# Performance work log

Measured on AMD Instinct MI355X. Metric: run time of the kernel, lower is better.

## Reference

```python
import jax, jax.numpy as jnp
import numpy as np

N_HEADS = 12
LN_EPS = 1e-12


def _attention(x, mask, wq, bq, wk, bk, wv, bv, wo, bo):
    # standard BERT self-attention block (QKV + output projection, no LN here)
    B, S, D = x.shape
    Dh = D // N_HEADS
    q = (x @ wq + bq).reshape(B, S, N_HEADS, Dh)
    k = (x @ wk + bk).reshape(B, S, N_HEADS, Dh)
    v = (x @ wv + bv).reshape(B, S, N_HEADS, Dh)
    scores = jnp.einsum('bqhd,bkhd->bhqk', q, k) / jnp.sqrt(jnp.asarray(Dh, x.dtype))
    scores = scores + mask[:, None, None, :]  # additive mask, broadcast over heads/queries
    a = jax.nn.softmax(scores, axis=-1)
    ctx = jnp.einsum('bhqk,bkhd->bqhd', a, v).reshape(B, S, D)
    return ctx @ wo + bo


def _ffn(x, w1, b1, w2, b2):
    return jax.nn.gelu(x @ w1 + b1, approximate=False) @ w2 + b2


def _switch_ffn(x, wr, br, w1, b1, w2, b2):
    # token-level top-1 Switch FFN: route each token, scale output by max route prob.
    # All sub-experts are computed densely and combined with a one-hot mask so the
    # math is identical to gather/scatter dispatch but jit-friendly.
    B, S, D = x.shape
    E = wr.shape[-1]
    tok = x.reshape(-1, D)  # [N, D]
    p = jax.nn.softmax(tok @ wr + br, axis=-1)  # [N, E]
    pmax = p.max(axis=-1)
    oh = jax.nn.one_hot(p.argmax(axis=-1), E, dtype=tok.dtype)  # [N, E]
    h = jax.nn.gelu(jnp.einsum('nd,edf->enf', tok, w1) + b1[:, None, :], approximate=False)
    y = jnp.einsum('enf,efd->end', h, w2) + b2[:, None, :]  # [E, N, D]
    out = jnp.einsum('ne,end->nd', oh, y) * pmax[:, None]
    return out.reshape(B, S, D)


def setup_inputs() -> dict:
    B, S, D, F, U, E = 16, 128, 768, 3072, 4, 4
    key = jax.random.key(0)
    ks = jax.random.split(key, 20)
    w = lambda i, sh: jax.random.normal(ks[i], sh, dtype=jnp.float32) * 0.02
    z = lambda sh: jnp.zeros(sh, jnp.float32)
    return {
        'x': jax.random.normal(ks[0], (B, S, D), jnp.float32),
        'attn_mask': z((B, S)),
        'sw_w': w(1, (D, U)), 'sw_b': z((U,)),
        'ca_wq': w(2, (D, D)), 'ca_bq': z((D,)),
        'ca_wk': w(3, (D, D)), 'ca_bk': z((D,)),
        'ca_wv': w(4, (D, D)), 'ca_bv': z((D,)),
        'ca_wo': w(5, (D, D)), 'ca_bo': z((D,)),
        'ua_wq': w(6, (U, D, D)), 'ua_bq': z((U, D)),
        'ua_wk': w(7, (U, D, D)), 'ua_bk': z((U, D)),
        'ua_wv': w(8, (U, D, D)), 'ua_bv': z((U, D)),
        'ua_wo': w(9, (U, D, D)), 'ua_bo': z((U, D)),
        'cf_w1': w(10, (D, F)), 'cf_b1': z((F,)),
        'cf_w2': w(11, (F, D)), 'cf_b2': z((D,)),
        'ur_w': w(12, (U, D, E)), 'ur_b': z((U, E)),
        'uf_w1': w(13, (U, E, D, F)), 'uf_b1': z((U, E, F)),
        'uf_w2': w(14, (U, E, F, D)), 'uf_b2': z((U, E, D)),
        'ln_g': jnp.ones((D,), jnp.float32), 'ln_b': z((D,)),
    }


def reference(x, attn_mask, sw_w, sw_b,
              ca_wq, ca_bq, ca_wk, ca_bk, ca_wv, ca_bv, ca_wo, ca_bo,
              ua_wq, ua_bq, ua_wk, ua_bk, ua_wv, ua_bv, ua_wo, ua_bo,
              cf_w1, cf_b1, cf_w2, cf_b2,
              ur_w, ur_b, uf_w1, uf_b1, uf_w2, uf_b2,
              ln_g, ln_b):
    U = sw_w.shape[-1]
    # common attention expert (full batch)
    common_attn = _attention(x, attn_mask, ca_wq, ca_bq, ca_wk, ca_bk, ca_wv, ca_bv, ca_wo, ca_bo)
    # batch-level routing: mean-pool over sequence, softmax + top-1
    route_p = jax.nn.softmax(x.mean(axis=1) @ sw_w + sw_b, axis=-1)  # [B, U]
    pmax = route_p.max(axis=-1)    # [B]
    routes = route_p.argmax(axis=-1)  # [B]
    # unique attention experts: masked dense compute == gather/scatter by batch row
    unique_attn = jnp.zeros_like(x)
    for i in range(U):
        sel = (routes == i)[:, None, None]
        out_i = _attention(x, attn_mask, ua_wq[i], ua_bq[i], ua_wk[i], ua_bk[i],
                           ua_wv[i], ua_bv[i], ua_wo[i], ua_bo[i])
        unique_attn = unique_attn + jnp.where(sel, out_i, jnp.zeros((), x.dtype))
    # note: original multiplies ONLY the unique branch by route_prob_max
    att = common_attn + pmax[:, None, None] * unique_attn
    # unique Switch-FFN experts (token-level top-1 inside each unique expert)
    unique_ffn = jnp.zeros_like(x)
    for i in range(U):
        sel = (routes == i)[:, None, None]
        out_i = _switch_ffn(att, ur_w[i], ur_b[i], uf_w1[i], uf_b1[i], uf_w2[i], uf_b2[i])
        unique_ffn = unique_ffn + jnp.where(sel, out_i, jnp.zeros((), x.dtype))
    common_ffn = _ffn(att, cf_w1, cf_b1, cf_w2, cf_b2)
    ffn_out = common_ffn + unique_ffn  # dropout in eval mode == identity
    y = att + ffn_out
    mu = y.mean(axis=-1, keepdims=True)
    var = y.var(axis=-1, keepdims=True)
    return (y - mu) / jnp.sqrt(var + LN_EPS) * ln_g + ln_b
```

## Files before the change

kernel.cpp:

```cpp
#include <hip/hip_runtime.h>

#define NT 2048
#define Dm 768
#define Fm 3072
#define Bm 16
#define Sm 128
#define Hm 12
#define DHm 64

#define BM 64
#define BN 128
#define BK 32

typedef __attribute__((ext_vector_type(8))) short bf16x8;
typedef __attribute__((ext_vector_type(4))) float f32x4;

__device__ __forceinline__ unsigned short f2bf(float f){
  unsigned u = __float_as_uint(f);
  unsigned r = (u + 0x7fffu + ((u>>16)&1u)) >> 16;
  return (unsigned short)r;
}
__device__ __forceinline__ float bf2f(unsigned short h){ return __uint_as_float(((unsigned)h)<<16); }
__device__ __forceinline__ unsigned fsplit2(float x){
  unsigned short h = f2bf(x);
  unsigned short l = f2bf(x - bf2f(h));
  return (unsigned)h | ((unsigned)l << 16);
}
__device__ __forceinline__ float gelu_f(float x){
  return 0.5f*x*(1.0f + erff(x*0.70710678118654752f));
}

__device__ __forceinline__ void mm_tile(
    const short* __restrict__ Abf, int lda,
    const int* __restrict__ gidx, int m0, int mbound,
    const float* __restrict__ W0, int N, int K, int n0,
    f32x4 acc[2][4])
{
  int lane = threadIdx.x & 63, wv = threadIdx.x >> 6;
  int wm = wv & 1, wn = wv >> 1;
  int oct = lane >> 4, l16 = lane & 15;
  const short* aptr[2];
  #pragma unroll
  for(int fi=0; fi<2; fi++){
    int lr = wm*32 + fi*16 + l16;
    int grow = (lr < mbound) ? (gidx ? gidx[m0 + lr] : (m0 + lr)) : -1;
    aptr[fi] = (grow >= 0) ? (Abf + (size_t)grow*lda + oct*8) : nullptr;
  }
  const float* bptr[4];
  #pragma unroll
  for(int fj=0; fj<4; fj++)
    bptr[fj] = W0 + (size_t)(oct*8)*N + (n0 + wn*64 + fj*16 + l16);

  const bf16x8 zz = {0,0,0,0,0,0,0,0};
  bf16x8 av[2]; float bw[4][8];
  #pragma unroll
  for(int fi=0; fi<2; fi++) av[fi] = aptr[fi] ? *(const bf16x8*)(aptr[fi]) : zz;
  #pragma unroll
  for(int fj=0; fj<4; fj++)
    #pragma unroll
    for(int i=0;i<8;i++) bw[fj][i] = bptr[fj][(size_t)i*N];

  for(int k0=0; k0<K; k0+=BK){
    bf16x8 af[2]; af[0]=av[0]; af[1]=av[1];
    bf16x8 bfr[4];
    #pragma unroll
    for(int fj=0; fj<4; fj++)
      #pragma unroll
      for(int i=0;i<8;i++) bfr[fj][i] = (short)f2bf(bw[fj][i]);
    if(k0+BK < K){
      int kn = k0 + BK;
      #pragma unroll
      for(int fi=0; fi<2; fi++) av[fi] = aptr[fi] ? *(const bf16x8*)(aptr[fi] + kn) : zz;
      #pragma unroll
      for(int fj=0; fj<4; fj++)
        #pragma unroll
        for(int i=0;i<8;i++) bw[fj][i] = bptr[fj][(size_t)(kn + i)*N];
    }
    #pragma unroll
    for(int fi=0; fi<2; fi++)
      #pragma unroll
      for(int fj=0; fj<4; fj++)
        acc[fi][fj] = __builtin_amdgcn_mfma_f32_16x16x32_bf16(af[fi], bfr[fj], acc[fi][fj], 0, 0, 0);
  }
}

__device__ __forceinline__ void mm_tile3b(
    const short* __restrict__ Ahi, const short* __restrict__ Alo, int lda, int m0, int acol,
    const float* __restrict__ W0, int N, int K, int n0,
    f32x4 acc[2][4])
{
  int lane = threadIdx.x & 63, wv = threadIdx.x >> 6;
  int wm = wv & 1, wn = wv >> 1;
  int oct = lane >> 4, l16 = lane & 15;
  size_t aoffs[2];
  #pragma unroll
  for(int fi=0; fi<2; fi++){
    int lr = wm*32 + fi*16 + l16;
    aoffs[fi] = (size_t)(m0 + lr)*lda + acol + oct*8;
  }
  const float* bptr[4];
  #pragma unroll
  for(int fj=0; fj<4; fj++)
    bptr[fj] = W0 + (size_t)(oct*8)*N + (n0 + wn*64 + fj*16 + l16);

  bf16x8 avH[2], avL[2]; float bw[4][8];
  #pragma unroll
  for(int fi=0; fi<2; fi++){
    avH[fi] = *(const bf16x8*)(Ahi + aoffs[fi]);
    avL[fi] = *(const bf16x8*)(Alo + aoffs[fi]);
  }
  #pragma unroll
  for(int fj=0; fj<4; fj++)
    #pragma unroll
    for(int i=0;i<8;i++) bw[fj][i] = bptr[fj][(size_t)i*N];

  for(int k0=0; k0<K; k0+=BK){
    bf16x8 ah[2], al[2];
    #pragma unroll
    for(int fi=0; fi<2; fi++){ ah[fi]=avH[fi]; al[fi]=avL[fi]; }
    bf16x8 bh[4], bl[4];
    #pragma unroll
    for(int fj=0; fj<4; fj++)
      #pragma unroll
      for(int i=0;i<8;i++){
        unsigned p = fsplit2(bw[fj][i]);
        bh[fj][i] = (short)(p & 0xffff);
        bl[fj][i] = (short)(p >> 16);
      }
    if(k0+BK < K){
      int kn = k0 + BK;
      #pragma unroll
      for(int fi=0; fi<2; fi++){
        avH[fi] = *(const bf16x8*)(Ahi + aoffs[fi] + kn);
        avL[fi] = *(const bf16x8*)(Alo + aoffs[fi] + kn);
      }
      #pragma unroll
      for(int fj=0; fj<4; fj++)
        #pragma unroll
        for(int i=0;i<8;i++) bw[fj][i] = bptr[fj][(size_t)(kn + i)*N];
    }
    #pragma unroll
    for(int fi=0; fi<2; fi++)
      #pragma unroll
      for(int fj=0; fj<4; fj++){
        acc[fi][fj] = __builtin_amdgcn_mfma_f32_16x16x32_bf16(ah[fi], bh[fj], acc[fi][fj], 0, 0, 0);
        acc[fi][fj] = __builtin_amdgcn_mfma_f32_16x16x32_bf16(ah[fi], bl[fj], acc[fi][fj], 0, 0, 0);
        acc[fi][fj] = __builtin_amdgcn_mfma_f32_16x16x32_bf16(al[fi], bh[fj], acc[fi][fj], 0, 0, 0);
      }
  }
}

__global__ __launch_bounds__(256) void k_split_x(const float* __restrict__ in,
    short* __restrict__ hi, short* __restrict__ lo, int n4){
  int i = blockIdx.x*256 + threadIdx.x;
  if(i < n4){
    float4 v = ((const float4*)in)[i];
    unsigned p0 = fsplit2(v.x), p1 = fsplit2(v.y), p2 = fsplit2(v.z), p3 = fsplit2(v.w);
    short4 h, l;
    h.x=(short)(p0&0xffff); l.x=(short)(p0>>16);
    h.y=(short)(p1&0xffff); l.y=(short)(p1>>16);
    h.z=(short)(p2&0xffff); l.z=(short)(p2>>16);
    h.w=(short)(p3&0xffff); l.w=(short)(p3>>16);
    ((short4*)hi)[i] = h;
    ((short4*)lo)[i] = l;
  }
}

struct PtrArr6 { const float* w[6]; const float* b[6]; };

__global__ __launch_bounds__(256) void mm3_qkv(const short* __restrict__ x_hi,
    const short* __restrict__ x_lo, PtrArr6 pa,
    const int* __restrict__ routeb, float* __restrict__ qkvout)
{
  int n0 = blockIdx.x*BN, m0 = blockIdx.y*BM, z = blockIdx.z;
  int bidx = m0 >> 7;
  const float* W = pa.w[z]; const float* bias = pa.b[z];
  if(z >= 3){ int e = routeb[bidx]; W += (size_t)e*Dm*Dm; bias += (size_t)e*Dm; }
  f32x4 acc[2][4] = {};
  mm_tile3b(x_hi, x_lo, Dm, m0, 0, W, Dm, Dm, n0, acc);
  float* outp = qkvout + (size_t)z*NT*Dm;
  int lane = threadIdx.x&63, wv = threadIdx.x>>6, wm = wv&1, wn = wv>>1;
  #pragma unroll
  for(int fi=0; fi<2; fi++)
    #pragma unroll
    for(int fj=0; fj<4; fj++)
      #pragma unroll
      for(int r=0; r<4; r++){
        int row = m0 + wm*32 + fi*16 + ((lane>>4)<<2) + r;
        int col = n0 + wn*64 + fj*16 + (lane&15);
        outp[(size_t)row*Dm + col] = acc[fi][fj][r] + bias[col];
      }
}

__global__ __launch_bounds__(256) void mm3_outproj(const short* __restrict__ ctx_hi,
    const short* __restrict__ ctx_lo,
    const float* __restrict__ ca_wo, const float* __restrict__ ua_wo,
    const float* __restrict__ ca_bo, const float* __restrict__ ua_bo,
    const int* __restrict__ routeb, const float* __restrict__ pmaxb,
    float* __restrict__ att2)
{
  int n0 = blockIdx.x*BN, m0 = blockIdx.y*BM, kc = blockIdx.z;
  int bidx = m0 >> 7;
  int e = routeb[bidx];
  const float* W    = kc ? (ua_wo + (size_t)e*Dm*Dm) : ca_wo;
  const float* bias = kc ? (ua_bo + (size_t)e*Dm)    : ca_bo;
  float bscale = kc ? pmaxb[bidx] : 1.0f;
  f32x4 acc[2][4] = {};
  mm_tile3b(ctx_hi, ctx_lo, 1536, m0, kc*Dm, W, Dm, Dm, n0, acc);
  float* outp = att2 + (size_t)kc*NT*Dm;
  int lane = threadIdx.x&63, wv = threadIdx.x>>6, wm = wv&1, wn = wv>>1;
  #pragma unroll
  for(int fi=0; fi<2; fi++)
    #pragma unroll
    for(int fj=0; fj<4; fj++)
      #pragma unroll
      for(int r=0; r<4; r++){
        int row = m0 + wm*32 + fi*16 + ((lane>>4)<<2) + r;
        int col = n0 + wn*64 + fj*16 + (lane&15);
        outp[(size_t)row*Dm + col] = acc[fi][fj][r] + bscale*bias[col];
      }
}

__global__ __launch_bounds__(256) void k_att_sum(const float* __restrict__ att2,
    float* __restrict__ att, short* __restrict__ attbf, int n4){
  int i = blockIdx.x*256 + threadIdx.x;
  if(i < n4){
    const size_t P4 = (size_t)NT*Dm/4;
    float4 a = ((const float4*)att2)[i];
    float4 b = ((const float4*)att2)[P4 + i];
    float4 v; v.x=a.x+b.x; v.y=a.y+b.y; v.z=a.z+b.z; v.w=a.w+b.w;
    ((float4*)att)[i] = v;
    short4 o;
    o.x=(short)f2bf(v.x); o.y=(short)f2bf(v.y); o.z=(short)f2bf(v.z); o.w=(short)f2bf(v.w);
    ((short4*)attbf)[i] = o;
  }
}

__global__ __launch_bounds__(256) void mm_fstage(const short* __restrict__ attbf,
    const float* __restrict__ cf_w1, const float* __restrict__ cf_b1,
    const float* __restrict__ uf_w1, const float* __restrict__ uf_b1,
    const int* __restrict__ idxl, const int* __restrict__ gbase, const int* __restrict__ gcnt,
    const int* __restrict__ tlist, const int* __restrict__ ntl,
    short* __restrict__ h, short* __restrict__ hg)
{
  int n0 = blockIdx.x*BN, y = blockIdx.y;
  int lane = threadIdx.x&63, wv = threadIdx.x>>6, wm = wv&1, wn = wv>>1;
  f32x4 acc[2][4] = {};
  if(y < 32){
    int m0 = y*BM;
    mm_tile(attbf, Dm, nullptr, m0, BM, cf_w1, Fm, Dm, n0, acc);
    #pragma unroll
    for(int fi=0; fi<2; fi++)
      #pragma unroll
      for(int fj=0; fj<4; fj++)
        #pragma unroll
        for(int r=0; r<4; r++){
          int row = m0 + wm*32 + fi*16 + ((lane>>4)<<2) + r;
          int col = n0 + wn*64 + fj*16 + (lane&15);
          h[(size_t)row*Fm + col] = (short)f2bf(gelu_f(acc[fi][fj][r] + cf_b1[col]));
        }
  } else {
    int i = y - 32;
    if(i >= ntl[0]) return;
    int v = tlist[i], g = v>>8, t = v&255;
    int cnt = gcnt[g], r0 = t*BM, pos0 = gbase[g] + r0;
    mm_tile(attbf, Dm, idxl, pos0, cnt - r0, uf_w1 + (size_t)g*Dm*Fm, Fm, Dm, n0, acc);
    const float* bias = uf_b1 + (size_t)g*Fm;
    #pragma unroll
    for(int fi=0; fi<2; fi++)
      #pragma unroll
      for(int fj=0; fj<4; fj++)
        #pragma unroll
        for(int r=0; r<4; r++){
          int lr = wm*32 + fi*16 + ((lane>>4)<<2) + r;
          if(r0 + lr >= cnt) continue;
          int col = n0 + wn*64 + fj*16 + (lane&15);
          hg[(size_t)(pos0+lr)*Fm + col] = (short)f2bf(gelu_f(acc[fi][fj][r] + bias[col]));
        }
  }
}

__global__ __launch_bounds__(256) void mm_dstage(const short* __restrict__ h,
    const short* __restrict__ hg,
    const float* __restrict__ cf_w2, const float* __restrict__ cf_b2,
    const float* __restrict__ uf_w2, const float* __restrict__ uf_b2,
    const int* __restrict__ idxl, const int* __restrict__ gbase, const int* __restrict__ gcnt,
    const int* __restrict__ tlist, const int* __restrict__ ntl,
    const float* __restrict__ tokp, short* __restrict__ ycf4, short* __restrict__ yuo4)
{
  const int KC = Fm/4;
  int n0 = blockIdx.x*BN, y = blockIdx.y, kc = blockIdx.z;
  int lane = threadIdx.x&63, wv = threadIdx.x>>6, wm = wv&1, wn = wv>>1;
  f32x4 acc[2][4] = {};
  if(y < 32){
    int m0 = y*BM;
    mm_tile(h + kc*KC, Fm, nullptr, m0, BM, cf_w2 + (size_t)kc*KC*Dm, Dm, KC, n0, acc);
    short* outp = ycf4 + (size_t)kc*NT*Dm;
    #pragma unroll
    for(int fi=0; fi<2; fi++)
      #pragma unroll
      for(int fj=0; fj<4; fj++)
        #pragma unroll
        for(int r=0; r<4; r++){
          int row = m0 + wm*32 + fi*16 + ((lane>>4)<<2) + r;
          int col = n0 + wn*64 + fj*16 + (lane&15);
          outp[(size_t)row*Dm + col] = (short)f2bf(acc[fi][fj][r] + (kc==0 ? cf_b2[col] : 0.f));
        }
  } else {
    int i = y - 32;
    if(i >= ntl[0]) return;
    int v = tlist[i], g = v>>8, t = v&255;
    int cnt = gcnt[g], r0 = t*BM, pos0 = gbase[g] + r0;
    mm_tile(hg + kc*KC, Fm, nullptr, pos0, cnt - r0,
            uf_w2 + (size_t)g*Fm*Dm + (size_t)kc*KC*Dm, Dm, KC, n0, acc);
    const float* bias = uf_b2 + (size_t)g*Dm;
    short* outp = yuo4 + (size_t)kc*NT*Dm;
    #pragma unroll
    for(int fi=0; fi<2; fi++)
      #pragma unroll
      for(int fj=0; fj<4; fj++)
        #pragma unroll
        for(int r=0; r<4; r++){
          int lr = wm*32 + fi*16 + ((lane>>4)<<2) + r;
          int rm = (r0 + lr < cnt) ? idxl[pos0 + lr] : -1;
          if(rm < 0) continue;
          int col = n0 + wn*64 + fj*16 + (lane&15);
          float vv = acc[fi][fj][r] + (kc==0 ? bias[col] : 0.f);
          outp[(size_t)rm*Dm + col] = (short)f2bf(vv * tokp[rm]);
        }
  }
}

__global__ __launch_bounds__(256) void k_route_batch(const float* __restrict__ xf,
    const float* __restrict__ sw_w, const float* __restrict__ sw_b,
    float* __restrict__ pmax_b, int* __restrict__ route_b){
  int b = blockIdx.x, tid = threadIdx.x;
  __shared__ float xm[Dm];
  for(int d=tid; d<Dm; d+=256){
    float s=0.f;
    const float* xp = xf + ((size_t)b*Sm)*Dm + d;
    for(int ss=0; ss<Sm; ss++) s += xp[(size_t)ss*Dm];
    xm[d] = s*(1.0f/Sm);
  }
  __syncthreads();
  float a0=0,a1=0,a2=0,a3=0;
  for(int d=tid; d<Dm; d+=256){
    float xv = xm[d];
    a0 += xv*sw_w[d*4+0]; a1 += xv*sw_w[d*4+1];
    a2 += xv*sw_w[d*4+2]; a3 += xv*sw_w[d*4+3];
  }
  __shared__ float red[4][256];
  red[0][tid]=a0; red[1][tid]=a1; red[2][tid]=a2; red[3][tid]=a3;
  for(int off=128; off>0; off>>=1){
    __syncthreads();
    if(tid<off){ for(int u=0;u<4;u++) red[u][tid]+=red[u][tid+off]; }
  }
  __syncthreads();
  if(tid==0){
    float l[4]; for(int u=0;u<4;u++) l[u]=red[u][0]+sw_b[u];
    float m=l[0]; int arg=0;
    for(int u=1;u<4;u++) if(l[u]>m){ m=l[u]; arg=u; }
    float s=0; for(int u=0;u<4;u++) s+=expf(l[u]-m);
    pmax_b[b]=1.0f/s;
    route_b[b]=arg;
  }
}

__global__ __launch_bounds__(256) void k_attn_f(const float* __restrict__ qkv,
    const float* __restrict__ mask, const float* __restrict__ pmaxb,
    short* __restrict__ ctx_hi, short* __restrict__ ctx_lo)
{
  int h = blockIdx.x, b = blockIdx.y, z = blockIdx.z;
  int qh = z & 1, kind = z >> 1;
  const float* Q  = qkv + (size_t)(kind*3+0)*NT*Dm;
  const float* Kp = qkv + (size_t)(kind*3+1)*NT*Dm;
  const float* Vp = qkv + (size_t)(kind*3+2)*NT*Dm;
  int tid = threadIdx.x;
  __shared__ float kv[128][64];
  __shared__ float sS[64][128];
  size_t base = ((size_t)b*Sm)*Dm + h*DHm;
  for(int l=tid; l<2048; l+=256){
    int s=l>>4, d0=(l&15)*4;
    float4 v = *(const float4*)(Kp + base + (size_t)s*Dm + d0);
    kv[s][d0]=v.x; kv[s][d0+1]=v.y; kv[s][d0+2]=v.z; kv[s][d0+3]=v.w;
  }
  __syncthreads();
  int ql = tid>>2, quarter = tid&3;
  int qi = qh*64 + ql;
  float qreg[64];
  const float* qp = Q + base + (size_t)qi*Dm;
  #pragma unroll
  for(int d=0; d<64; d++) qreg[d] = qp[d];
  int kb = quarter*32;
  for(int ki=kb; ki<kb+32; ki++){
    float s=0.f;
    #pragma unroll
    for(int d=0; d<64; d++) s += qreg[d]*kv[ki][d];
    sS[ql][ki] = s*0.125f + mask[b*Sm+ki];
  }
  __syncthreads();
  if(tid < 64){
    float m = -3.4e38f;
    for(int ki=0; ki<128; ki++) m = fmaxf(m, sS[tid][ki]);
    float sum = 0.f;
    for(int ki=0; ki<128; ki++){ float e = expf(sS[tid][ki]-m); sS[tid][ki]=e; sum+=e; }
    float inv = 1.0f/sum;
    for(int ki=0; ki<128; ki++) sS[tid][ki] *= inv;
  }
  __syncthreads();
  for(int l=tid; l<2048; l+=256){
    int s=l>>4, d0=(l&15)*4;
    float4 v = *(const float4*)(Vp + base + (size_t)s*Dm + d0);
    kv[s][d0]=v.x; kv[s][d0+1]=v.y; kv[s][d0+2]=v.z; kv[s][d0+3]=v.w;
  }
  __syncthreads();
  float sc = kind ? pmaxb[b] : 1.0f;
  int d0 = quarter*16;
  for(int d=d0; d<d0+16; d++){
    float s=0.f;
    for(int ki=0; ki<128; ki++) s += sS[ql][ki]*kv[ki][d];
    float v = s*sc;
    size_t idx = ((size_t)b*Sm + qi)*1536 + kind*Dm + h*DHm + d;
    unsigned short hh = f2bf(v);
    ctx_hi[idx] = (short)hh;
    ctx_lo[idx] = (short)f2bf(v - bf2f(hh));
  }
}

__global__ __launch_bounds__(256) void k_tok_route(const float* __restrict__ att,
    const float* __restrict__ ur_w, const float* __restrict__ ur_b,
    const int* __restrict__ route_b, float* __restrict__ tok_pmax,
    int* __restrict__ tok_e, int* __restrict__ grp_count)
{
  int n = blockIdx.x, tid = threadIdx.x;
  int i = route_b[n>>7];
  const float* w = ur_w + (size_t)i*Dm*4;
  const float* ap = att + (size_t)n*Dm;
  float a0=0,a1=0,a2=0,a3=0;
  for(int d=tid; d<Dm; d+=256){
    float a = ap[d];
    a0 += a*w[d*4+0]; a1 += a*w[d*4+1];
    a2 += a*w[d*4+2]; a3 += a*w[d*4+3];
  }
  __shared__ float red[4][256];
  red[0][tid]=a0; red[1][tid]=a1; red[2][tid]=a2; red[3][tid]=a3;
  for(int off=128; off>0; off>>=1){
    __syncthreads();
    if(tid<off){ for(int u=0;u<4;u++) red[u][tid]+=red[u][tid+off]; }
  }
  __syncthreads();
  if(tid==0){
    float l[4]; for(int u=0;u<4;u++) l[u]=red[u][0]+ur_b[i*4+u];
    float m=l[0]; int arg=0;
    for(int u=1;u<4;u++) if(l[u]>m){ m=l[u]; arg=u; }
    float s=0; for(int u=0;u<4;u++) s+=expf(l[u]-m);
    tok_pmax[n] = 1.0f/s;
    tok_e[n] = arg;
    atomicAdd(&grp_count[i*4+arg], 1);
  }
}

__global__ void k_prefix(const int* __restrict__ cnt, int* __restrict__ base,
                         int* __restrict__ cur, int* __restrict__ tlist, int* __restrict__ ntl){
  if(threadIdx.x==0 && blockIdx.x==0){
    int s=0, nt=0;
    for(int g=0; g<16; g++){
      base[g]=s; cur[g]=s;
      int tg = (cnt[g] + BM - 1)/BM;
      for(int t=0; t<tg; t++){ if(nt<64) tlist[nt++] = (g<<8)|t; }
      s += cnt[g];
    }
    ntl[0] = nt;
  }
}

__global__ void k_scatter(const int* __restrict__ route_b, const int* __restrict__ tok_e,
                          int* __restrict__ cur, int* __restrict__ idxl){
  int n = blockIdx.x*256 + threadIdx.x;
  if(n < NT){
    int g = route_b[n>>7]*4 + tok_e[n];
    int pos = atomicAdd(&cur[g], 1);
    idxl[pos] = n;
  }
}

__global__ __launch_bounds__(256) void k_final_ln(const float* __restrict__ att,
    const short* __restrict__ ycf4, const short* __restrict__ yuo4,
    const float* __restrict__ ln_g, const float* __restrict__ ln_b, float* __restrict__ out)
{
  int n = blockIdx.x, tid = threadIdx.x;
  __shared__ float yb[Dm];
  __shared__ float red[256];
  size_t base = (size_t)n*Dm;
  const size_t P = (size_t)NT*Dm;
  float ps = 0.f;
  for(int d=tid; d<Dm; d+=256){
    float v = att[base+d];
    #pragma unroll
    for(int c=0; c<4; c++){
      v += bf2f((unsigned short)ycf4[c*P + base + d]);
      v += bf2f((unsigned short)yuo4[c*P + base + d]);
    }
    yb[d]=v; ps+=v;
  }
  red[tid]=ps;
  for(int off=128; off>0; off>>=1){ __syncthreads(); if(tid<off) red[tid]+=red[tid+off]; }
  __syncthreads();
  float mu = red[0]*(1.0f/Dm);
  __syncthreads();
  float pv = 0.f;
  for(int d=tid; d<Dm; d+=256){ float t = yb[d]-mu; pv += t*t; }
  red[tid]=pv;
  for(int off=128; off>0; off>>=1){ __syncthreads(); if(tid<off) red[tid]+=red[tid+off]; }
  __syncthreads();
  float var = red[0]*(1.0f/Dm);
  float rstd = rsqrtf(var + 1e-12f);
  for(int d=tid; d<Dm; d+=256){
    out[base+d] = (yb[d]-mu)*rstd*ln_g[d] + ln_b[d];
  }
}

extern "C" void kernel_launch(void* const* d_in, const int* in_sizes, int n_in,
                              void* d_out, int out_size, void* d_ws, size_t ws_size,
                              hipStream_t stream)
{
  const float* x     =(const float*)d_in[0];
  const float* mask  =(const float*)d_in[1];
  const float* sw_w  =(const float*)d_in[2];
  const float* sw_b  =(const float*)d_in[3];
  const float* ca_wq =(const float*)d_in[4];
  const float* ca_bq =(const float*)d_in[5];
  const float* ca_wk =(const float*)d_in[6];
  const float* ca_bk =(const float*)d_in[7];
  const float* ca_wv =(const float*)d_in[8];
  const float* ca_bv =(const float*)d_in[9];
  const float* ca_wo =(const float*)d_in[10];
  const float* ca_bo =(const float*)d_in[11];
  const float* ua_wq =(const float*)d_in[12];
  const float* ua_bq =(const float*)d_in[13];
  const float* ua_wk =(const float*)d_in[14];
  const float* ua_bk =(const float*)d_in[15];
  const float* ua_wv =(const float*)d_in[16];
  const float* ua_bv =(const float*)d_in[17];
  const float* ua_wo =(const float*)d_in[18];
  const float* ua_bo =(const float*)d_in[19];
  const float* cf_w1 =(const float*)d_in[20];
  const float* cf_b1 =(const float*)d_in[21];
  const float* cf_w2 =(const float*)d_in[22];
  const float* cf_b2 =(const float*)d_in[23];
  const float* ur_w  =(const float*)d_in[24];
  const float* ur_b  =(const float*)d_in[25];
  const float* uf_w1 =(const float*)d_in[26];
  const float* uf_b1 =(const float*)d_in[27];
  const float* uf_w2 =(const float*)d_in[28];
  const float* uf_b2 =(const float*)d_in[29];
  const float* ln_g  =(const float*)d_in[30];
  const float* ln_b  =(const float*)d_in[31];

  float* region = (float*)d_ws;
  float* qkv    = region;
  short* ctx_hi = (short*)(region + (size_t)6*NT*Dm);
  short* ctx_lo = (short*)(region + (size_t)7*NT*Dm);
  float* att2   = region;
  short* h_bf   = (short*)region;
  short* hg_bf  = (short*)region + (size_t)NT*Fm;
  short* ycf4   = (short*)(region + (size_t)4*NT*Dm);
  short* yuo4   = (short*)(region + (size_t)6*NT*Dm);
  float* fp     = region + (size_t)8*NT*Dm;
  short* x_hi   = (short*)fp;
  short* x_lo   = x_hi + (size_t)NT*Dm;
  float* att    = fp; fp += (size_t)NT*Dm;
  float* tokp   = fp; fp += NT;
  float* pmaxb  = fp; fp += 16;
  short* att_bf = (short*)fp;
  int*   ip     = (int*)(att_bf + (size_t)NT*Dm);
  int* routeb = ip; ip += 16;
  int* toke   = ip; ip += NT;
  int* gcnt   = ip; ip += 16;
  int* gbase  = ip; ip += 16;
  int* gcur   = ip; ip += 16;
  int* idxl   = ip; ip += NT;
  int* tlist  = ip; ip += 64;
  int* ntl    = ip; ip += 1;
  size_t need = (size_t)((char*)ip - (char*)d_ws);
  if(need > ws_size) return;

  (void)hipMemsetAsync(gcnt, 0, 16*sizeof(int), stream);

  k_route_batch<<<16, 256, 0, stream>>>(x, sw_w, sw_b, pmaxb, routeb);
  k_split_x<<<(NT*Dm/4 + 255)/256, 256, 0, stream>>>(x, x_hi, x_lo, NT*Dm/4);

  PtrArr6 pa;
  pa.w[0]=ca_wq; pa.w[1]=ca_wk; pa.w[2]=ca_wv; pa.w[3]=ua_wq; pa.w[4]=ua_wk; pa.w[5]=ua_wv;
  pa.b[0]=ca_bq; pa.b[1]=ca_bk; pa.b[2]=ca_bv; pa.b[3]=ua_bq; pa.b[4]=ua_bk; pa.b[5]=ua_bv;
  mm3_qkv<<<dim3(Dm/BN, NT/BM, 6), 256, 0, stream>>>(x_hi, x_lo, pa, routeb, qkv);

  k_attn_f<<<dim3(Hm, Bm, 4), 256, 0, stream>>>(qkv, mask, pmaxb, ctx_hi, ctx_lo);

  mm3_outproj<<<dim3(Dm/BN, NT/BM, 2), 256, 0, stream>>>(ctx_hi, ctx_lo, ca_wo, ua_wo,
                                                         ca_bo, ua_bo, routeb, pmaxb, att2);
  k_att_sum<<<(NT*Dm/4 + 255)/256, 256, 0, stream>>>(att2, att, att_bf, NT*Dm/4);

  k_tok_route<<<NT, 256, 0, stream>>>(att, ur_w, ur_b, routeb, tokp, toke, gcnt);
  k_prefix<<<1, 64, 0, stream>>>(gcnt, gbase, gcur, tlist, ntl);
  k_scatter<<<NT/256, 256, 0, stream>>>(routeb, toke, gcur, idxl);

  mm_fstage<<<dim3(Fm/BN, 32+48), 256, 0, stream>>>(att_bf, cf_w1, cf_b1, uf_w1, uf_b1,
                                                    idxl, gbase, gcnt, tlist, ntl, h_bf, hg_bf);

  mm_dstage<<<dim3(Dm/BN, 32+48, 4), 256, 0, stream>>>(h_bf, hg_bf, cf_w2, cf_b2, uf_w2, uf_b2,
                                                       idxl, gbase, gcnt, tlist, ntl, tokp,
                                                       ycf4, yuo4);

  k_final_ln<<<NT, 256, 0, stream>>>(att, ycf4, yuo4, ln_g, ln_b, (float*)d_out);
}
```

Baseline: 678.7 us.

## Keep attention scores in registers with shuffle softmax and vectorized LDS access

The attention kernel drops the shared score matrix. Each thread now keeps its 32 scores in registers, computes the softmax max and sum with cross-lane shuffles among the four threads of a query, and accumulates a partial P·V over its strided keys before a shuffle reduction. K/V tiles are padded to 68 columns and read and written as float4, and outputs are stored as short4. This removes the serial 64-thread softmax and cuts LDS traffic and barriers, in exchange for higher register pressure from the 64-float accumulator and 32 scores.

```diff
diff --git a/kernel.cpp b/kernel.cpp
--- a/kernel.cpp
+++ b/kernel.cpp
@@ -376,54 +376,85 @@
   const float* Kp = qkv + (size_t)(kind*3+1)*NT*Dm;
   const float* Vp = qkv + (size_t)(kind*3+2)*NT*Dm;
   int tid = threadIdx.x;
-  __shared__ float kv[128][64];
-  __shared__ float sS[64][128];
+  __shared__ float kv[128][68];
   size_t base = ((size_t)b*Sm)*Dm + h*DHm;
   for(int l=tid; l<2048; l+=256){
-    int s=l>>4, d0=(l&15)*4;
-    float4 v = *(const float4*)(Kp + base + (size_t)s*Dm + d0);
-    kv[s][d0]=v.x; kv[s][d0+1]=v.y; kv[s][d0+2]=v.z; kv[s][d0+3]=v.w;
-  }
-  __syncthreads();
+    int s=l>>4, d4=(l&15)*4;
+    *(float4*)&kv[s][d4] = *(const float4*)(Kp + base + (size_t)s*Dm + d4);
+  }
   int ql = tid>>2, quarter = tid&3;
   int qi = qh*64 + ql;
-  float qreg[64];
+  float4 q4[16];
   const float* qp = Q + base + (size_t)qi*Dm;
   #pragma unroll
-  for(int d=0; d<64; d++) qreg[d] = qp[d];
-  int kb = quarter*32;
-  for(int ki=kb; ki<kb+32; ki++){
+  for(int j=0;j<16;j++) q4[j] = *(const float4*)(qp + j*4);
+  __syncthreads();
+  float sc[32];
+  #pragma unroll 4
+  for(int t=0;t<32;t++){
+    int ki = quarter + 4*t;
     float s=0.f;
     #pragma unroll
-    for(int d=0; d<64; d++) s += qreg[d]*kv[ki][d];
-    sS[ql][ki] = s*0.125f + mask[b*Sm+ki];
-  }
-  __syncthreads();
-  if(tid < 64){
-    float m = -3.4e38f;
-    for(int ki=0; ki<128; ki++) m = fmaxf(m, sS[tid][ki]);
-    float sum = 0.f;
-    for(int ki=0; ki<128; ki++){ float e = expf(sS[tid][ki]-m); sS[tid][ki]=e; sum+=e; }
-    float inv = 1.0f/sum;
-    for(int ki=0; ki<128; ki++) sS[tid][ki] *= inv;
-  }
+    for(int j=0;j<16;j++){
+      float4 k4 = *(float4*)&kv[ki][j*4];
+      s += q4[j].x*k4.x + q4[j].y*k4.y + q4[j].z*k4.z + q4[j].w*k4.w;
+    }
+    sc[t] = s*0.125f + mask[b*Sm+ki];
+  }
+  float m = sc[0];
+  #pragma unroll
+  for(int t=1;t<32;t++) m = fmaxf(m, sc[t]);
+  m = fmaxf(m, __shfl_xor(m,1));
+  m = fmaxf(m, __shfl_xor(m,2));
+  float sum = 0.f;
+  #pragma unroll
+  for(int t=0;t<32;t++){ sc[t] = expf(sc[t]-m); sum += sc[t]; }
+  sum += __shfl_xor(sum,1);
+  sum += __shfl_xor(sum,2);
+  float inv = 1.0f/sum;
+  #pragma unroll
+  for(int t=0;t<32;t++) sc[t] *= inv;
   __syncthreads();
   for(int l=tid; l<2048; l+=256){
-    int s=l>>4, d0=(l&15)*4;
-    float4 v = *(const float4*)(Vp + base + (size_t)s*Dm + d0);
-    kv[s][d0]=v.x; kv[s][d0+1]=v.y; kv[s][d0+2]=v.z; kv[s][d0+3]=v.w;
-  }
-  __syncthreads();
-  float sc = kind ? pmaxb[b] : 1.0f;
-  int d0 = quarter*16;
-  for(int d=d0; d<d0+16; d++){
-    float s=0.f;
-    for(int ki=0; ki<128; ki++) s += sS[ql][ki]*kv[ki][d];
-    float v = s*sc;
-    size_t idx = ((size_t)b*Sm + qi)*1536 + kind*Dm + h*DHm + d;
-    unsigned short hh = f2bf(v);
-    ctx_hi[idx] = (short)hh;
-    ctx_lo[idx] = (short)f2bf(v - bf2f(hh));
+    int s=l>>4, d4=(l&15)*4;
+    *(float4*)&kv[s][d4] = *(const float4*)(Vp + base + (size_t)s*Dm + d4);
+  }
+  __syncthreads();
+  float4 part[16];
+  #pragma unroll
+  for(int j=0;j<16;j++){ part[j].x=0; part[j].y=0; part[j].z=0; part[j].w=0; }
+  #pragma unroll 4
+  for(int t=0;t<32;t++){
+    int ki = quarter + 4*t;
+    float p = sc[t];
+    #pragma unroll
+    for(int j=0;j<16;j++){
+      float4 v4 = *(float4*)&kv[ki][j*4];
+      part[j].x += p*v4.x; part[j].y += p*v4.y; part[j].z += p*v4.z; part[j].w += p*v4.w;
+    }
+  }
+  #pragma unroll
+  for(int j=0;j<16;j++){
+    part[j].x += __shfl_xor(part[j].x,1); part[j].x += __shfl_xor(part[j].x,2);
+    part[j].y += __shfl_xor(part[j].y,1); part[j].y += __shfl_xor(part[j].y,2);
+    part[j].z += __shfl_xor(part[j].z,1); part[j].z += __shfl_xor(part[j].z,2);
+    part[j].w += __shfl_xor(part[j].w,1); part[j].w += __shfl_xor(part[j].w,2);
+  }
+  float sck = kind ? pmaxb[b] : 1.0f;
+  size_t obase = ((size_t)b*Sm + qi)*1536 + kind*Dm + h*DHm;
+  #pragma unroll
+  for(int jj=0;jj<4;jj++){
+    int j = quarter*4 + jj;
+    float4 v = part[j];
+    v.x *= sck; v.y *= sck; v.z *= sck; v.w *= sck;
+    short4 hh, ll;
+    unsigned short t0;
+    t0=f2bf(v.x); hh.x=(short)t0; ll.x=(short)f2bf(v.x-bf2f(t0));
+    t0=f2bf(v.y); hh.y=(short)t0; ll.y=(short)f2bf(v.y-bf2f(t0));
+    t0=f2bf(v.z); hh.z=(short)t0; ll.z=(short)f2bf(v.z-bf2f(t0));
+    t0=f2bf(v.w); hh.w=(short)t0; ll.w=(short)f2bf(v.w-bf2f(t0));
+    *(short4*)(ctx_hi + obase + j*4) = hh;
+    *(short4*)(ctx_lo + obase + j*4) = ll;
   }
 }
 
```

Result: faster. 602.8 us (-11.2%).
